# Kernel optimization log

Measured on AMD Instinct MI355X. Metric: run time of the kernel, lower is better.

The kernel has to match this reference:

```python
import jax, jax.numpy as jnp
import numpy as np

N_SRC = 100_000
N_DST = 100_000
N_EDGES = 1_600_000
D_IN = 256
N_HEADS = 4
OUT_FEATS = 32
NEG_SLOPE = 0.2


def setup_inputs() -> dict:
    key = jax.random.key(0)
    k1, k2, k3, k4, k5, k6, k7 = jax.random.split(key, 7)
    return {
        "feat_src": jax.random.normal(k1, (N_SRC, D_IN), dtype=jnp.float32),
        "feat_dst": jax.random.normal(k2, (N_DST, D_IN), dtype=jnp.float32),
        "w_src": jax.random.normal(k3, (D_IN, N_HEADS * OUT_FEATS), dtype=jnp.float32) * 0.05,
        "w_dst": jax.random.normal(k4, (D_IN, N_HEADS * OUT_FEATS), dtype=jnp.float32) * 0.05,
        "attn": jax.random.normal(k5, (N_HEADS, 2 * OUT_FEATS), dtype=jnp.float32) * 0.05,
        "src_idx": jax.random.randint(k6, (N_EDGES,), 0, N_SRC, dtype=jnp.int32),
        "dst_idx": jax.random.randint(k7, (N_EDGES,), 0, N_DST, dtype=jnp.int32),
    }


def reference(feat_src, feat_dst, w_src, w_dst, attn, src_idx, dst_idx):
    H, two_d = attn.shape
    D = two_d // 2
    n_dst = feat_dst.shape[0]
    # node transformations (dropout rate = 0.0 -> identity)
    fs = (feat_src @ w_src).reshape(-1, H, D)   # [Ns, H, D]
    fd = (feat_dst @ w_dst).reshape(-1, H, D)   # [Nd, H, D]
    # per-node attention logits: e_dst uses first half, e_src second half
    e_dst = (fd * attn[:, :D]).sum(-1)          # [Nd, H]
    e_src = (fs * attn[:, D:]).sum(-1)          # [Ns, H]
    # u_add_v on edges + leaky relu
    e = e_src[src_idx] + e_dst[dst_idx]         # [E, H]
    e = jnp.where(e > 0, e, NEG_SLOPE * e)
    # edge softmax: segment softmax over incoming edges of each dst node
    m = jax.ops.segment_max(e, dst_idx, num_segments=n_dst)       # [Nd, H]
    m = jnp.where(jnp.isfinite(m), m, 0.0)                        # empty segments
    ex = jnp.exp(e - m[dst_idx])                                  # [E, H]
    denom = jax.ops.segment_sum(ex, dst_idx, num_segments=n_dst)  # [Nd, H]
    a = ex / denom[dst_idx]                                       # [E, H]
    # u_mul_e + sum aggregation
    msg = fs[src_idx] * a[:, :, None]                             # [E, H, D]
    out = jax.ops.segment_sum(msg, dst_idx, num_segments=n_dst)   # [Nd, H, D]
    return jax.nn.relu(out.reshape(n_dst, H * D))
```

## Files before the change

kernel.cpp:

```cpp
#include <hip/hip_runtime.h>

#define N_NODES 100000
#define N_EDGES 1600000
#define D_IN    256
#define HD      128
#define NEG_SLOPE 0.2f

#define BUK_SH    5
#define BUK_NODES 32
#define NBUCKETS ((N_NODES + BUK_NODES - 1) / BUK_NODES)
#define BUK_CAP  1024
#define BUK_CH   8192
#define NB_BUK   ((N_EDGES + BUK_CH - 1) / BUK_CH)

#define NB_GEMM ((N_NODES + 255) / 256)
#define NB_EDST 1024
#define NB_ZERO ((NBUCKETS + 255) / 256)

typedef __bf16 bf16x8 __attribute__((ext_vector_type(8)));
typedef float  f32x4  __attribute__((ext_vector_type(4)));

__device__ __forceinline__ float lrelu_exp(float v) {
  v = v > 0.f ? v : NEG_SLOPE * v;
  return __expf(v);
}
__device__ __forceinline__ float bf_lo(unsigned u) { return __uint_as_float(u << 16); }
__device__ __forceinline__ float bf_hi(unsigned u) { return __uint_as_float(u & 0xffff0000u); }

__global__ __launch_bounds__(256) void prep_kernel(const float* __restrict__ w_src,
                                                   const float* __restrict__ w_dst,
                                                   const float* __restrict__ attn,
                                                   ushort* __restrict__ wT,
                                                   float* __restrict__ v_dst,
                                                   int* __restrict__ bcur) {
  int bid = blockIdx.x;
  int tid = threadIdx.x;
  if (bid < 128) {
    int idx = bid * 256 + tid;
    int k = idx >> 7, n = idx & 127;
    __bf16 bv = (__bf16)w_src[idx];
    wT[n * 256 + k] = *(const ushort*)&bv;
  } else if (bid == 128) {
    int k = tid;
    for (int h = 0; h < 4; ++h) {
      float s = 0.f;
      for (int d = 0; d < 32; ++d)
        s += w_dst[k * HD + h * 32 + d] * attn[h * 64 + d];
      v_dst[k * 4 + h] = s;
    }
  } else {
    int i = (bid - 129) * 256 + tid;
    if (i < NBUCKETS) bcur[i] = 0;
  }
}

__global__ __launch_bounds__(1024) void gemm_kernel(const float* __restrict__ A,
                                                    const ushort* __restrict__ wT16,
                                                    const float* __restrict__ attn,
                                                    unsigned* __restrict__ fs16,
                                                    float* __restrict__ e_src,
                                                    int M) {
  __shared__ ushort Bl[128 * 256];
  const int bid = blockIdx.x;
  const int tid = threadIdx.x;
  const int lane = tid & 63, wid = tid >> 6;
  const int lr = lane & 15, hi = lane >> 4;

  {
    const uint4* wg4 = (const uint4*)wT16;
#pragma unroll
    for (int i = 0; i < 4; ++i) {
      int c = i * 1024 + tid;
      int col = c >> 5;
      unsigned byte = ((unsigned)c * 16u) ^ (((unsigned)col & 31u) << 4);
      *(uint4*)((char*)Bl + byte) = wg4[c];
    }
  }

  f32x4 acc[8];
  const f32x4 zf = {0.f, 0.f, 0.f, 0.f};
#pragma unroll
  for (int n = 0; n < 8; ++n) acc[n] = zf;

  const int bm = bid * 256;
  int row0 = bm + wid * 16 + lr;
  int row0c = row0 < M ? row0 : M - 1;
  const float* a0p = A + (size_t)row0c * D_IN;

  __syncthreads();

#pragma unroll
  for (int ks = 0; ks < 8; ++ks) {
    const int ko = ks * 32 + hi * 8;
    float4 u0 = *(const float4*)(a0p + ko);
    float4 u1 = *(const float4*)(a0p + ko + 4);
    bf16x8 af0;
    af0[0] = (__bf16)u0.x; af0[1] = (__bf16)u0.y; af0[2] = (__bf16)u0.z; af0[3] = (__bf16)u0.w;
    af0[4] = (__bf16)u1.x; af0[5] = (__bf16)u1.y; af0[6] = (__bf16)u1.z; af0[7] = (__bf16)u1.w;
    bf16x8 bf[8];
#pragma unroll
    for (int n = 0; n < 8; ++n) {
      unsigned col = (unsigned)(n * 16 + lr);
      unsigned byte = (col * 512u + (unsigned)(ks * 64 + hi * 16)) ^ ((col & 31u) << 4);
      bf[n] = *(const bf16x8*)((const char*)Bl + byte);
    }
#pragma unroll
    for (int n = 0; n < 8; ++n)
      acc[n] = __builtin_amdgcn_mfma_f32_16x16x32_bf16(af0, bf[n], acc[n], 0, 0, 0);
  }

#pragma unroll
  for (int n = 0; n < 8; ++n) {
#pragma unroll
    for (int r4 = 0; r4 < 4; ++r4) {
      float val = acc[n][r4];
      float pv  = __shfl_xor(val, 1, 64);
      int gr = bm + wid * 16 + hi * 4 + r4;
      if (!(lane & 1) && gr < M) {
        __bf16 b0 = (__bf16)val, b1 = (__bf16)pv;
        unsigned pk = ((unsigned)*(const ushort*)&b1 << 16) | *(const ushort*)&b0;
        fs16[(size_t)gr * 64 + n * 8 + (lr >> 1)] = pk;
      }
    }
  }

#pragma unroll
  for (int gh = 0; gh < 4; ++gh) {
    float av0 = attn[gh * 64 + 32 + lr];
    float av1 = attn[gh * 64 + 48 + lr];
#pragma unroll
    for (int r4 = 0; r4 < 4; ++r4) {
      float s = acc[2 * gh][r4] * av0 + acc[2 * gh + 1][r4] * av1;
      s += __shfl_xor(s, 1, 64);
      s += __shfl_xor(s, 2, 64);
      s += __shfl_xor(s, 4, 64);
      s += __shfl_xor(s, 8, 64);
      int gr = bm + wid * 16 + hi * 4 + r4;
      if (lr == 0 && gr < M) e_src[(size_t)gr * 4 + gh] = s;
    }
  }
}

__global__ __launch_bounds__(256) void edst_kernel(const float* __restrict__ feat_dst,
                                                   const float* __restrict__ v_dst,
                                                   float* __restrict__ e_dst) {
  __shared__ float4 vds[256];
  const int tid = threadIdx.x;
  vds[tid] = ((const float4*)v_dst)[tid];
  __syncthreads();
  const int l = tid & 15;
  const int grp = tid >> 4;
  for (int n = blockIdx.x * 16 + grp; n < N_NODES; n += NB_EDST * 16) {
    const float* fp = feat_dst + (size_t)n * D_IN;
    float ax = 0.f, ay = 0.f, az = 0.f, aw = 0.f;
#pragma unroll
    for (int c = 0; c < 4; ++c) {
      const int k0 = c * 64 + l * 4;
      float4 f = *(const float4*)(fp + k0);
      float4 v0 = vds[k0 + 0], v1 = vds[k0 + 1], v2 = vds[k0 + 2], v3 = vds[k0 + 3];
      ax = fmaf(f.x, v0.x, fmaf(f.y, v1.x, fmaf(f.z, v2.x, fmaf(f.w, v3.x, ax))));
      ay = fmaf(f.x, v0.y, fmaf(f.y, v1.y, fmaf(f.z, v2.y, fmaf(f.w, v3.y, ay))));
      az = fmaf(f.x, v0.z, fmaf(f.y, v1.z, fmaf(f.z, v2.z, fmaf(f.w, v3.z, az))));
      aw = fmaf(f.x, v0.w, fmaf(f.y, v1.w, fmaf(f.z, v2.w, fmaf(f.w, v3.w, aw))));
    }
#pragma unroll
    for (int off = 1; off < 16; off <<= 1) {
      ax += __shfl_xor(ax, off, 64);
      ay += __shfl_xor(ay, off, 64);
      az += __shfl_xor(az, off, 64);
      aw += __shfl_xor(aw, off, 64);
    }
    if (l == 0) *(float4*)(e_dst + (size_t)n * 4) = make_float4(ax, ay, az, aw);
  }
}

__global__ __launch_bounds__(1024) void bucket_kernel(const int* __restrict__ src,
                                                      const int* __restrict__ dstv,
                                                      int* __restrict__ bcur,
                                                      unsigned* __restrict__ ebuk) {
  __shared__ int bh[NBUCKETS];
  const int tid = threadIdx.x;
  const int e0 = blockIdx.x * BUK_CH;
  for (int j = tid; j < NBUCKETS; j += 1024) bh[j] = 0;
  __syncthreads();
  for (int i = tid; i < BUK_CH; i += 1024) {
    int e = e0 + i;
    if (e < N_EDGES) atomicAdd(&bh[dstv[e] >> BUK_SH], 1);
  }
  __syncthreads();
  for (int j = tid; j < NBUCKETS; j += 1024) {
    int c = bh[j];
    bh[j] = (c > 0) ? atomicAdd(&bcur[j], c) : 0;
  }
  __syncthreads();
  for (int i = tid; i < BUK_CH; i += 1024) {
    int e = e0 + i;
    if (e < N_EDGES) {
      int d = dstv[e];
      int b = d >> BUK_SH;
      int p = atomicAdd(&bh[b], 1);
      if (p < BUK_CAP)
        ebuk[(size_t)b * BUK_CAP + p] =
            ((unsigned)src[e] << BUK_SH) | (unsigned)(d & (BUK_NODES - 1));
    }
  }
}

__global__ __launch_bounds__(256) void agg_kernel(const unsigned* __restrict__ ebuk,
                                                  const int* __restrict__ bcur,
                                                  const float4* __restrict__ e_src,
                                                  const float4* __restrict__ e_dst,
                                                  const unsigned* __restrict__ fs16,
                                                  float* __restrict__ out, int N) {
  __shared__ unsigned sorted_e[BUK_CAP];
  __shared__ int lcnt[BUK_NODES];
  __shared__ int lofs_s[BUK_NODES + 1];
  __shared__ int lcur[BUK_NODES];
  __shared__ float sh_ex[4][4][72];
  const int tid = threadIdx.x;
  const int wslot = tid >> 6;
  const int lane = tid & 63;
  const int lo = blockIdx.x * BUK_NODES;
  const size_t start = (size_t)blockIdx.x * BUK_CAP;
  const int cnt_e = min(bcur[blockIdx.x], BUK_CAP);

  if (tid < BUK_NODES) lcnt[tid] = 0;
  __syncthreads();
  for (int i = tid; i < cnt_e; i += 256)
    atomicAdd(&lcnt[ebuk[start + i] & (BUK_NODES - 1)], 1);
  __syncthreads();
  if (tid == 0) {
    int run = 0;
    for (int j = 0; j < BUK_NODES; ++j) {
      lofs_s[j] = run; lcur[j] = run; run += lcnt[j];
    }
    lofs_s[BUK_NODES] = run;
  }
  __syncthreads();
  for (int i = tid; i < cnt_e; i += 256) {
    unsigned e = ebuk[start + i];
    int p = atomicAdd(&lcur[e & (BUK_NODES - 1)], 1);
    sorted_e[p] = e;
  }
  __syncthreads();

  const int g = lane >> 4;
  const int q = lane & 15;
  const int h = q >> 2;

  for (int nl = wslot * 8; nl < wslot * 8 + 8; ++nl) {
    int node = lo + nl;
    if (node >= N) break;
    const int nb = lofs_s[nl], ne = lofs_s[nl + 1];
    const float4 ed = e_dst[node];
    float a0=0.f,a1=0.f,a2=0.f,a3=0.f,a4=0.f,a5=0.f,a6=0.f,a7=0.f,den=0.f;

    for (int cb = nb; cb < ne; cb += 64) {
      int cs = min(64, ne - cb);
      if (lane < cs) {
        unsigned ent = sorted_e[cb + lane];
        int s = (int)(ent >> BUK_SH);
        float4 a = e_src[s];
        sh_ex[wslot][0][lane] = lrelu_exp(a.x + ed.x);
        sh_ex[wslot][1][lane] = lrelu_exp(a.y + ed.y);
        sh_ex[wslot][2][lane] = lrelu_exp(a.z + ed.z);
        sh_ex[wslot][3][lane] = lrelu_exp(a.w + ed.w);
      }
      __threadfence_block();
      int j = 0;
      for (; j + 4 <= cs; j += 4) {
        int e = j + g;
        int s = (int)(sorted_e[cb + e] >> BUK_SH);
        float ex = sh_ex[wslot][h][e];
        uint4 u = *(const uint4*)(fs16 + (size_t)s * 64 + q * 4);
        a0 = fmaf(ex, bf_lo(u.x), a0); a1 = fmaf(ex, bf_hi(u.x), a1);
        a2 = fmaf(ex, bf_lo(u.y), a2); a3 = fmaf(ex, bf_hi(u.y), a3);
        a4 = fmaf(ex, bf_lo(u.z), a4); a5 = fmaf(ex, bf_hi(u.z), a5);
        a6 = fmaf(ex, bf_lo(u.w), a6); a7 = fmaf(ex, bf_hi(u.w), a7);
        den += ex;
      }
      if (j < cs) {
        int e = j + g;
        bool pred = e < cs;
        int ec = pred ? e : 0;
        int s = (int)(sorted_e[cb + ec] >> BUK_SH);
        float ex = pred ? sh_ex[wslot][h][ec] : 0.f;
        uint4 u = *(const uint4*)(fs16 + (size_t)s * 64 + q * 4);
        a0 = fmaf(ex, bf_lo(u.x), a0); a1 = fmaf(ex, bf_hi(u.x), a1);
        a2 = fmaf(ex, bf_lo(u.y), a2); a3 = fmaf(ex, bf_hi(u.y), a3);
        a4 = fmaf(ex, bf_lo(u.z), a4); a5 = fmaf(ex, bf_hi(u.z), a5);
        a6 = fmaf(ex, bf_lo(u.w), a6); a7 = fmaf(ex, bf_hi(u.w), a7);
        den += ex;
      }
      __threadfence_block();
    }

    den += __shfl_xor(den, 16, 64); den += __shfl_xor(den, 32, 64);
    a0 += __shfl_xor(a0, 16, 64); a0 += __shfl_xor(a0, 32, 64);
    a1 += __shfl_xor(a1, 16, 64); a1 += __shfl_xor(a1, 32, 64);
    a2 += __shfl_xor(a2, 16, 64); a2 += __shfl_xor(a2, 32, 64);
    a3 += __shfl_xor(a3, 16, 64); a3 += __shfl_xor(a3, 32, 64);
    a4 += __shfl_xor(a4, 16, 64); a4 += __shfl_xor(a4, 32, 64);
    a5 += __shfl_xor(a5, 16, 64); a5 += __shfl_xor(a5, 32, 64);
    a6 += __shfl_xor(a6, 16, 64); a6 += __shfl_xor(a6, 32, 64);
    a7 += __shfl_xor(a7, 16, 64); a7 += __shfl_xor(a7, 32, 64);
    if (lane < 16) {
      float inv = den > 0.f ? 1.f / den : 0.f;
      float4 o1, o2;
      o1.x = fmaxf(a0 * inv, 0.f); o1.y = fmaxf(a1 * inv, 0.f);
      o1.z = fmaxf(a2 * inv, 0.f); o1.w = fmaxf(a3 * inv, 0.f);
      o2.x = fmaxf(a4 * inv, 0.f); o2.y = fmaxf(a5 * inv, 0.f);
      o2.z = fmaxf(a6 * inv, 0.f); o2.w = fmaxf(a7 * inv, 0.f);
      float* op = out + (size_t)node * HD + q * 8;
      *(float4*)(op)     = o1;
      *(float4*)(op + 4) = o2;
    }
  }
}

extern "C" void kernel_launch(void* const* d_in, const int* in_sizes, int n_in,
                              void* d_out, int out_size, void* d_ws, size_t ws_size,
                              hipStream_t stream) {
  const float* feat_src = (const float*)d_in[0];
  const float* feat_dst = (const float*)d_in[1];
  const float* w_src    = (const float*)d_in[2];
  const float* w_dst    = (const float*)d_in[3];
  const float* attn     = (const float*)d_in[4];
  const int*   src_idx  = (const int*)d_in[5];
  const int*   dst_idx  = (const int*)d_in[6];
  float* out = (float*)d_out;
  char* ws = (char*)d_ws;

  unsigned* fs16  = (unsigned*)(ws);
  float*    e_src = (float*)(ws + 25600000);
  float*    e_dst = (float*)(ws + 27200000);
  unsigned* ebuk  = (unsigned*)(ws + 28800000);
  float*    v_dst = (float*)(ws + 41600000);
  ushort*   wT16  = (ushort*)(ws + 41604096);
  int*      bcur  = (int*)  (ws + 41669632);

  prep_kernel<<<129 + NB_ZERO, 256, 0, stream>>>(w_src, w_dst, attn, wT16, v_dst, bcur);

  gemm_kernel<<<NB_GEMM, 1024, 0, stream>>>(feat_src, wT16, attn, fs16, e_src, N_NODES);

  edst_kernel<<<NB_EDST, 256, 0, stream>>>(feat_dst, v_dst, e_dst);

  bucket_kernel<<<NB_BUK, 1024, 0, stream>>>(src_idx, dst_idx, bcur, ebuk);

  agg_kernel<<<NBUCKETS, 256, 0, stream>>>(ebuk, bcur,
      (const float4*)e_src, (const float4*)e_dst, fs16, out, N_NODES);
}
```

Measured before the change: 178.6 us.

## Precompute edge attention weights per bucket and unroll gather loop four edges deep

Edge exponentials for the whole bucket are now computed once by all 256 threads into a shared array before aggregation, instead of per-wavefront 64-edge chunks with fences. The aggregation loop then processes 16 edges per iteration, issuing four independent feature gathers per lane to raise memory-level parallelism. This costs more shared memory (about 16KB extra) and an extra block barrier, which may reduce occupancy.

```diff
diff --git a/kernel.cpp b/kernel.cpp
--- a/kernel.cpp
+++ b/kernel.cpp
@@ -16,6 +16,8 @@
 #define NB_GEMM ((N_NODES + 255) / 256)
 #define NB_EDST 1024
 #define NB_ZERO ((NBUCKETS + 255) / 256)
+
+#define EX_STRIDE 1032
 
 typedef __bf16 bf16x8 __attribute__((ext_vector_type(8)));
 typedef float  f32x4  __attribute__((ext_vector_type(4)));
@@ -213,10 +215,10 @@
                                                   const unsigned* __restrict__ fs16,
                                                   float* __restrict__ out, int N) {
   __shared__ unsigned sorted_e[BUK_CAP];
+  __shared__ float ex_s[4][EX_STRIDE];
   __shared__ int lcnt[BUK_NODES];
   __shared__ int lofs_s[BUK_NODES + 1];
   __shared__ int lcur[BUK_NODES];
-  __shared__ float sh_ex[4][4][72];
   const int tid = threadIdx.x;
   const int wslot = tid >> 6;
   const int lane = tid & 63;
@@ -244,6 +246,19 @@
   }
   __syncthreads();
 
+  for (int i = tid; i < cnt_e; i += 256) {
+    unsigned ent = sorted_e[i];
+    int s  = (int)(ent >> BUK_SH);
+    int dl = (int)(ent & (BUK_NODES - 1));
+    float4 a  = e_src[s];
+    float4 ed = e_dst[lo + dl];
+    ex_s[0][i] = lrelu_exp(a.x + ed.x);
+    ex_s[1][i] = lrelu_exp(a.y + ed.y);
+    ex_s[2][i] = lrelu_exp(a.z + ed.z);
+    ex_s[3][i] = lrelu_exp(a.w + ed.w);
+  }
+  __syncthreads();
+
   const int g = lane >> 4;
   const int q = lane & 15;
   const int h = q >> 2;
@@ -252,47 +267,41 @@
     int node = lo + nl;
     if (node >= N) break;
     const int nb = lofs_s[nl], ne = lofs_s[nl + 1];
-    const float4 ed = e_dst[node];
     float a0=0.f,a1=0.f,a2=0.f,a3=0.f,a4=0.f,a5=0.f,a6=0.f,a7=0.f,den=0.f;
 
-    for (int cb = nb; cb < ne; cb += 64) {
-      int cs = min(64, ne - cb);
-      if (lane < cs) {
-        unsigned ent = sorted_e[cb + lane];
-        int s = (int)(ent >> BUK_SH);
-        float4 a = e_src[s];
-        sh_ex[wslot][0][lane] = lrelu_exp(a.x + ed.x);
-        sh_ex[wslot][1][lane] = lrelu_exp(a.y + ed.y);
-        sh_ex[wslot][2][lane] = lrelu_exp(a.z + ed.z);
-        sh_ex[wslot][3][lane] = lrelu_exp(a.w + ed.w);
-      }
-      __threadfence_block();
-      int j = 0;
-      for (; j + 4 <= cs; j += 4) {
-        int e = j + g;
-        int s = (int)(sorted_e[cb + e] >> BUK_SH);
-        float ex = sh_ex[wslot][h][e];
-        uint4 u = *(const uint4*)(fs16 + (size_t)s * 64 + q * 4);
-        a0 = fmaf(ex, bf_lo(u.x), a0); a1 = fmaf(ex, bf_hi(u.x), a1);
-        a2 = fmaf(ex, bf_lo(u.y), a2); a3 = fmaf(ex, bf_hi(u.y), a3);
-        a4 = fmaf(ex, bf_lo(u.z), a4); a5 = fmaf(ex, bf_hi(u.z), a5);
-        a6 = fmaf(ex, bf_lo(u.w), a6); a7 = fmaf(ex, bf_hi(u.w), a7);
-        den += ex;
-      }
-      if (j < cs) {
-        int e = j + g;
-        bool pred = e < cs;
-        int ec = pred ? e : 0;
-        int s = (int)(sorted_e[cb + ec] >> BUK_SH);
-        float ex = pred ? sh_ex[wslot][h][ec] : 0.f;
-        uint4 u = *(const uint4*)(fs16 + (size_t)s * 64 + q * 4);
-        a0 = fmaf(ex, bf_lo(u.x), a0); a1 = fmaf(ex, bf_hi(u.x), a1);
-        a2 = fmaf(ex, bf_lo(u.y), a2); a3 = fmaf(ex, bf_hi(u.y), a3);
-        a4 = fmaf(ex, bf_lo(u.z), a4); a5 = fmaf(ex, bf_hi(u.z), a5);
-        a6 = fmaf(ex, bf_lo(u.w), a6); a7 = fmaf(ex, bf_hi(u.w), a7);
-        den += ex;
-      }
-      __threadfence_block();
+    for (int cb = nb; cb < ne; cb += 16) {
+      int e0 = cb + g, e1 = e0 + 4, e2 = e0 + 8, e3 = e0 + 12;
+      bool p0 = e0 < ne, p1 = e1 < ne, p2 = e2 < ne, p3 = e3 < ne;
+      int c0 = p0 ? e0 : nb, c1 = p1 ? e1 : nb, c2 = p2 ? e2 : nb, c3 = p3 ? e3 : nb;
+      int s0 = (int)(sorted_e[c0] >> BUK_SH);
+      int s1 = (int)(sorted_e[c1] >> BUK_SH);
+      int s2 = (int)(sorted_e[c2] >> BUK_SH);
+      int s3 = (int)(sorted_e[c3] >> BUK_SH);
+      uint4 u0 = *(const uint4*)(fs16 + (size_t)s0 * 64 + q * 4);
+      uint4 u1 = *(const uint4*)(fs16 + (size_t)s1 * 64 + q * 4);
+      uint4 u2 = *(const uint4*)(fs16 + (size_t)s2 * 64 + q * 4);
+      uint4 u3 = *(const uint4*)(fs16 + (size_t)s3 * 64 + q * 4);
+      float x0 = p0 ? ex_s[h][c0] : 0.f;
+      float x1 = p1 ? ex_s[h][c1] : 0.f;
+      float x2 = p2 ? ex_s[h][c2] : 0.f;
+      float x3 = p3 ? ex_s[h][c3] : 0.f;
+      a0 = fmaf(x0, bf_lo(u0.x), a0); a1 = fmaf(x0, bf_hi(u0.x), a1);
+      a2 = fmaf(x0, bf_lo(u0.y), a2); a3 = fmaf(x0, bf_hi(u0.y), a3);
+      a4 = fmaf(x0, bf_lo(u0.z), a4); a5 = fmaf(x0, bf_hi(u0.z), a5);
+      a6 = fmaf(x0, bf_lo(u0.w), a6); a7 = fmaf(x0, bf_hi(u0.w), a7);
+      a0 = fmaf(x1, bf_lo(u1.x), a0); a1 = fmaf(x1, bf_hi(u1.x), a1);
+      a2 = fmaf(x1, bf_lo(u1.y), a2); a3 = fmaf(x1, bf_hi(u1.y), a3);
+      a4 = fmaf(x1, bf_lo(u1.z), a4); a5 = fmaf(x1, bf_hi(u1.z), a5);
+      a6 = fmaf(x1, bf_lo(u1.w), a6); a7 = fmaf(x1, bf_hi(u1.w), a7);
+      a0 = fmaf(x2, bf_lo(u2.x), a0); a1 = fmaf(x2, bf_hi(u2.x), a1);
+      a2 = fmaf(x2, bf_lo(u2.y), a2); a3 = fmaf(x2, bf_hi(u2.y), a3);
+      a4 = fmaf(x2, bf_lo(u2.z), a4); a5 = fmaf(x2, bf_hi(u2.z), a5);
+      a6 = fmaf(x2, bf_lo(u2.w), a6); a7 = fmaf(x2, bf_hi(u2.w), a7);
+      a0 = fmaf(x3, bf_lo(u3.x), a0); a1 = fmaf(x3, bf_hi(u3.x), a1);
+      a2 = fmaf(x3, bf_lo(u3.y), a2); a3 = fmaf(x3, bf_hi(u3.y), a3);
+      a4 = fmaf(x3, bf_lo(u3.z), a4); a5 = fmaf(x3, bf_hi(u3.z), a5);
+      a6 = fmaf(x3, bf_lo(u3.w), a6); a7 = fmaf(x3, bf_hi(u3.w), a7);
+      den += x0 + x1 + x2 + x3;
     }
 
     den += __shfl_xor(den, 16, 64); den += __shfl_xor(den, 32, 64);
```

Result: faster. 170.5 us (-4.5%).
